# Kernel tuning notes

Hardware: AMD Instinct MI355X
Metric: run time of the kernel (lower is better)

Reference implementation:

```python
import jax, jax.numpy as jnp
import numpy as np

MODES1 = 12
MODES2 = 12
IN_CH = 32
OUT_CH = 32
B, H, W = 16, 256, 256
SCALE = 1.0 / (IN_CH * OUT_CH)


def setup_inputs() -> dict:
    key = jax.random.key(0)
    k1, k2, k3 = jax.random.split(key, 3)
    x = jax.random.normal(k1, (B, IN_CH, H, W), dtype=jnp.float32)
    w1 = SCALE * jax.random.uniform(k2, (IN_CH, OUT_CH, MODES1, MODES2, 2), dtype=jnp.float32)
    w2 = SCALE * jax.random.uniform(k3, (IN_CH, OUT_CH, MODES1, MODES2, 2), dtype=jnp.float32)
    return {"x": x, "weights1": w1, "weights2": w2}


def _compl_mul2d(inp, w):
    # inp: [b,i,x,y] complex ; w: [i,o,x,y,2] real -> complex
    wc = jax.lax.complex(w[..., 0], w[..., 1])
    return jnp.einsum('bixy,ioxy->boxy', inp, wc)


def reference(x, weights1, weights2):
    H_, W_ = x.shape[-2], x.shape[-1]
    m1 = min(MODES1, H_ // 2)
    m2 = min(MODES2, W_ // 2 + 1)
    x_ft = jnp.fft.rfft2(x.astype(jnp.float32))  # [B, Cin, H, W//2+1]
    low = _compl_mul2d(x_ft[:, :, :m1, :m2], weights1[:, :, :m1, :m2])
    high = _compl_mul2d(x_ft[:, :, -m1:, :m2], weights2[:, :, :m1, :m2])
    out_ft = jnp.zeros((x.shape[0], OUT_CH, H_, W_ // 2 + 1), dtype=jnp.complex64)
    out_ft = out_ft.at[:, :, :m1, :m2].set(low)
    out_ft = out_ft.at[:, :, H_ - m1:, :m2].set(high)
    return jnp.fft.irfft2(out_ft, s=(H_, W_)).astype(x.dtype)
```

## Files before the change

kernel.cpp:

```cpp
#include <hip/hip_runtime.h>


#define TPI 6.28318530717958647692f

__global__ __launch_bounds__(256, 2) void k12_hwdft(const float* __restrict__ x,
                                                    float* __restrict__ Xf) {
  __shared__ float2 step2[128];
  __shared__ float red[4 * 7 * 128];
  __shared__ float2 Ys2[13 * 129];
  const int blk = blockIdx.x;
  const int bi = blk >> 1, wh = blk & 1;
  const int t = threadIdx.x;
  const int q = t >> 6, l = t & 63;

  if (t < 128) {
    float s, c;
    sincosf(TPI * (float)t * (1.0f / 256.0f), &s, &c);
    step2[t] = make_float2(c, s);
  }
  __syncthreads();

  const float2* xp2 = reinterpret_cast<const float2*>(x + (size_t)bi * 65536 + wh * 128) + l;
  float2 aC[13], aS12[12];
#pragma unroll
  for (int j = 0; j < 13; j++) aC[j] = make_float2(0.f, 0.f);
#pragma unroll
  for (int j = 0; j < 12; j++) aS12[j] = make_float2(0.f, 0.f);

  const int h0 = q * 32;
#pragma unroll 2
  for (int hh = 0; hh < 32; hh++) {
    int h = h0 + hh;
    float2 xa = xp2[h * 128];
    float2 xb = xp2[(h + 128) * 128];
    float2 xe = make_float2(xa.x + xb.x, xa.y + xb.y);
    float2 xo = make_float2(xa.x - xb.x, xa.y - xb.y);
    aC[0].x += xe.x; aC[0].y += xe.y;
    float2 st = step2[h];
    float cj = st.x, sj = st.y;
#pragma unroll
    for (int jj = 0; jj < 12; jj++) {
      float2 xj = (jj & 1) ? xe : xo;
      aC[jj + 1].x = fmaf(xj.x, cj, aC[jj + 1].x);
      aC[jj + 1].y = fmaf(xj.y, cj, aC[jj + 1].y);
      aS12[jj].x = fmaf(xj.x, sj, aS12[jj].x);
      aS12[jj].y = fmaf(xj.y, sj, aS12[jj].y);
      if (jj < 11) {
        float nc = fmaf(cj, st.x, -(sj * st.y));
        float ns = fmaf(cj, st.y, sj * st.x);
        cj = nc; sj = ns;
      }
    }
  }

  for (int p = 0; p < 4; p++) {
    __syncthreads();
#pragma unroll
    for (int cc = 0; cc < 7; cc++) {
      int cls = p * 7 + cc;
      if (cls < 26) {
        int j = cls >> 1;
        float2 v;
        if (cls & 1) v = (j == 0) ? make_float2(0.f, 0.f) : aS12[j - 1];
        else v = aC[j];
        *reinterpret_cast<float2*>(&red[(q * 7 + cc) * 128 + 2 * l]) = v;
      }
    }
    __syncthreads();
    for (int idx = t; idx < 7 * 128; idx += 256) {
      int cc = idx >> 7, wl = idx & 127;
      int cls = p * 7 + cc;
      if (cls < 26) {
        float s = red[(0 * 7 + cc) * 128 + wl] + red[(1 * 7 + cc) * 128 + wl] +
                  red[(2 * 7 + cc) * 128 + wl] + red[(3 * 7 + cc) * 128 + wl];
        if (cls & 1) Ys2[(cls >> 1) * 129 + wl].y = s;
        else         Ys2[(cls >> 1) * 129 + wl].x = s;
      }
    }
  }
  __syncthreads();

  if (t < 156) {
    int j = t / 12, kx = t % 12;
    float cs, ss;
    {
      float s, c;
      sincosf(TPI * (float)kx * (1.0f / 256.0f), &s, &c);
      cs = c; ss = -s;
    }
    const float2* CS = &Ys2[j * 129];
    float pr = 1.0f, pi = 0.0f;
    float A = 0, B = 0, D = 0, E = 0;
#pragma unroll 4
    for (int w = 0; w < 128; w++) {
      float2 v = CS[w];
      A = fmaf(v.x, pr, A);
      B = fmaf(v.x, pi, B);
      D = fmaf(v.y, pr, D);
      E = fmaf(v.y, pi, E);
      float npr = pr * cs - pi * ss;
      float npi = pr * ss + pi * cs;
      pr = npr; pi = npi;
    }
    float sgn = (wh && (kx & 1)) ? -1.0f : 1.0f;
    A *= sgn; B *= sgn; D *= sgn; E *= sgn;
    float2* Xo = reinterpret_cast<float2*>(Xf) + (size_t)wh * 147456;
    size_t base = (size_t)kx * 512 + bi;
    if (j <= 11) Xo[(size_t)j * 6144 + base] = make_float2(A + E, B - D);
    if (j >= 1)  Xo[(size_t)(24 - j) * 6144 + base] = make_float2(A - E, B + D);
  }
}

__global__ __launch_bounds__(256) void k3_mix(const float* __restrict__ Xf,
                                              const float* __restrict__ w1,
                                              const float* __restrict__ w2,
                                              float* __restrict__ Ff) {
  __shared__ float Xs[1024];
  __shared__ float Ws[2048];
  int m = blockIdx.x;
  int ky = m / 12, kx = m % 12;
  int t = threadIdx.x;
  const float* Xsl = Xf + (size_t)m * 1024;
  for (int e = t; e < 1024; e += 256) Xs[e] = Xsl[e] + Xsl[e + 294912];
  const float* Wp = (ky < 12) ? w1 : w2;
  int myr = (ky < 12) ? ky : ky - 12;
  int woff = myr * 24 + kx * 2;
  for (int e = t; e < 1024; e += 256) {
    float2 wv = *reinterpret_cast<const float2*>(Wp + (size_t)e * 288 + woff);
    Ws[e * 2] = wv.x; Ws[e * 2 + 1] = wv.y;
  }
  __syncthreads();
  int o = t & 31, bh = t >> 5;
  float ar = 0, ai = 0, br = 0, bi_ = 0;
#pragma unroll
  for (int i = 0; i < 32; i++) {
    float wr = Ws[i * 64 + o * 2], wi = Ws[i * 64 + o * 2 + 1];
    float x1r = Xs[bh * 64 + i * 2], x1i = Xs[bh * 64 + i * 2 + 1];
    float x2r = Xs[(bh + 8) * 64 + i * 2], x2i = Xs[(bh + 8) * 64 + i * 2 + 1];
    ar = fmaf(x1r, wr, ar); ar = fmaf(-x1i, wi, ar);
    ai = fmaf(x1r, wi, ai); ai = fmaf(x1i, wr, ai);
    br = fmaf(x2r, wr, br); br = fmaf(-x2i, wi, br);
    bi_ = fmaf(x2r, wi, bi_); bi_ = fmaf(x2i, wr, bi_);
  }
  float scale = (kx == 0 ? 1.0f : 2.0f) * (1.0f / 65536.0f);
  float2* Fo = reinterpret_cast<float2*>(Ff) + (size_t)m * 512;
  Fo[(size_t)bh * 32 + o] = make_float2(ar * scale, ai * scale);
  Fo[(size_t)(bh + 8) * 32 + o] = make_float2(br * scale, bi_ * scale);
}

__global__ __launch_bounds__(256) void k45_inv(const float* __restrict__ Ff,
                                               float* __restrict__ out) {
  __shared__ float tw[128 * 27];
  __shared__ float PQ[13 * 12 * 4];
  __shared__ float Gs[256 * 24];
  const int bo = blockIdx.x;
  const int t = threadIdx.x;
  const int l = t & 63, wq = t >> 6;

  for (int e = t; e < 128 * 13; e += 256) {
    int h = e / 13, j = e % 13;
    float s, c;
    sincosf(TPI * (float)((h * j) & 255) * (1.0f / 256.0f), &s, &c);
    tw[h * 27 + 2 * j] = c;
    tw[h * 27 + 2 * j + 1] = s;
  }
  if (t < 156) {
    int j = t / 12, kx = t % 12;
    const float2* F2 = reinterpret_cast<const float2*>(Ff);
    float lr = 0, li = 0, hr = 0, hi = 0;
    if (j < 12) { float2 v = F2[((size_t)j * 12 + kx) * 512 + bo]; lr = v.x; li = v.y; }
    if (j > 0)  { float2 v = F2[((size_t)(24 - j) * 12 + kx) * 512 + bo]; hr = v.x; hi = v.y; }
    PQ[(j * 12 + kx) * 4 + 0] = lr + hr;
    PQ[(j * 12 + kx) * 4 + 1] = li + hi;
    PQ[(j * 12 + kx) * 4 + 2] = hi - li;
    PQ[(j * 12 + kx) * 4 + 3] = lr - hr;
  }
  __syncthreads();

  if (t < 192) {
    const int kx = t % 12, hq = t / 12;
    float Pr[13], Pi[13], Qr[13], Qi[13];
#pragma unroll
    for (int j = 0; j < 13; j++) {
      Pr[j] = PQ[(j * 12 + kx) * 4 + 0];
      Pi[j] = PQ[(j * 12 + kx) * 4 + 1];
      Qr[j] = PQ[(j * 12 + kx) * 4 + 2];
      Qi[j] = PQ[(j * 12 + kx) * 4 + 3];
    }
    for (int hh = 0; hh < 8; hh++) {
      int h = hh * 16 + hq;
      float Er = 0, Ei = 0, Or = 0, Oi = 0;
#pragma unroll
      for (int j = 0; j < 13; j++) {
        float c = tw[h * 27 + 2 * j], s = tw[h * 27 + 2 * j + 1];
        if (j & 1) {
          Or = fmaf(Pr[j], c, Or); Or = fmaf(Qr[j], s, Or);
          Oi = fmaf(Pi[j], c, Oi); Oi = fmaf(Qi[j], s, Oi);
        } else {
          Er = fmaf(Pr[j], c, Er); Er = fmaf(Qr[j], s, Er);
          Ei = fmaf(Pi[j], c, Ei); Ei = fmaf(Qi[j], s, Ei);
        }
      }
      Gs[h * 24 + 2 * kx] = Er + Or;
      Gs[h * 24 + 2 * kx + 1] = Ei + Oi;
      Gs[(h + 128) * 24 + 2 * kx] = Er - Or;
      Gs[(h + 128) * 24 + 2 * kx + 1] = Ei - Oi;
    }
  }

  float cA[12], sA[12], cB[12], sB[12];
#pragma unroll
  for (int kx = 1; kx < 12; kx++) {
    float s, c;
    __sincosf(TPI * (float)((kx * (2 * l)) & 255) * (1.0f / 256.0f), &s, &c);
    cA[kx] = c; sA[kx] = s;
    __sincosf(TPI * (float)((kx * (2 * l + 1)) & 255) * (1.0f / 256.0f), &s, &c);
    cB[kx] = c; sB[kx] = s;
  }
  __syncthreads();

  float* ob0 = out + ((size_t)bo * 256 + wq * 64) * 256;
  for (int rs = 0; rs < 64; rs++) {
    int rl = wq * 64 + rs;
    float g[24];
    const float4* gr4 = reinterpret_cast<const float4*>(&Gs[rl * 24]);
#pragma unroll
    for (int qq = 0; qq < 6; qq++) {
      float4 v = gr4[qq];
      g[4 * qq] = v.x; g[4 * qq + 1] = v.y; g[4 * qq + 2] = v.z; g[4 * qq + 3] = v.w;
    }
    float E0 = g[0], O0 = 0, E1 = g[0], O1 = 0;
#pragma unroll
    for (int kx = 1; kx < 12; kx++) {
      float ta = g[2 * kx] * cA[kx] - g[2 * kx + 1] * sA[kx];
      float tb = g[2 * kx] * cB[kx] - g[2 * kx + 1] * sB[kx];
      if (kx & 1) { O0 += ta; O1 += tb; } else { E0 += ta; E1 += tb; }
    }
    float* orow = ob0 + rs * 256;
    *reinterpret_cast<float2*>(&orow[2 * l]) = make_float2(E0 + O0, E1 + O1);
    *reinterpret_cast<float2*>(&orow[128 + 2 * l]) = make_float2(E0 - O0, E1 - O1);
  }
}

extern "C" void kernel_launch(void* const* d_in, const int* in_sizes, int n_in,
                              void* d_out, int out_size, void* d_ws, size_t ws_size,
                              hipStream_t stream) {
  const float* x = (const float*)d_in[0];
  const float* w1 = (const float*)d_in[1];
  const float* w2 = (const float*)d_in[2];
  float* out = (float*)d_out;
  float* ws = (float*)d_ws;

  float* Xf = ws;
  float* Ff = ws + 589824;

  k12_hwdft<<<1024, 256, 0, stream>>>(x, Xf);
  k3_mix<<<288, 256, 0, stream>>>(Xf, w1, w2, Ff);
  k45_inv<<<512, 256, 0, stream>>>(Ff, out);
}
```

Measured before the change: 81.69 us.

## Split forward DFT kernel into four W-quarters per image with rotation fixup

The forward truncated-DFT kernel now gives each block a 64-column quarter of the W axis instead of a 128-column half. Each thread holds scalar accumulators instead of float2 pairs, and launch bounds rise to 4 blocks per CU. This doubles the grid to 2048 blocks and roughly halves registers per thread to raise occupancy and latency hiding on the load-bound pass. The quarter offset is applied as a twiddle rotation by multiples of i, and the mix kernel now sums four partial spectra, so it reads more and needs a larger workspace.

```diff
diff --git a/kernel.cpp b/kernel.cpp
--- a/kernel.cpp
+++ b/kernel.cpp
@@ -3,13 +3,13 @@
 
 #define TPI 6.28318530717958647692f
 
-__global__ __launch_bounds__(256, 2) void k12_hwdft(const float* __restrict__ x,
+__global__ __launch_bounds__(256, 4) void k12_hwdft(const float* __restrict__ x,
                                                     float* __restrict__ Xf) {
   __shared__ float2 step2[128];
-  __shared__ float red[4 * 7 * 128];
-  __shared__ float2 Ys2[13 * 129];
+  __shared__ float red[4 * 7 * 64];
+  __shared__ float2 Ys2[13 * 65];
   const int blk = blockIdx.x;
-  const int bi = blk >> 1, wh = blk & 1;
+  const int bi = blk >> 2, wq = blk & 3;
   const int t = threadIdx.x;
   const int q = t >> 6, l = t & 63;
 
@@ -20,31 +20,28 @@
   }
   __syncthreads();
 
-  const float2* xp2 = reinterpret_cast<const float2*>(x + (size_t)bi * 65536 + wh * 128) + l;
-  float2 aC[13], aS12[12];
-#pragma unroll
-  for (int j = 0; j < 13; j++) aC[j] = make_float2(0.f, 0.f);
-#pragma unroll
-  for (int j = 0; j < 12; j++) aS12[j] = make_float2(0.f, 0.f);
+  const float* xp = x + (size_t)bi * 65536 + wq * 64 + l;
+  float aC[13], aS12[12];
+#pragma unroll
+  for (int j = 0; j < 13; j++) aC[j] = 0.0f;
+#pragma unroll
+  for (int j = 0; j < 12; j++) aS12[j] = 0.0f;
 
   const int h0 = q * 32;
 #pragma unroll 2
   for (int hh = 0; hh < 32; hh++) {
     int h = h0 + hh;
-    float2 xa = xp2[h * 128];
-    float2 xb = xp2[(h + 128) * 128];
-    float2 xe = make_float2(xa.x + xb.x, xa.y + xb.y);
-    float2 xo = make_float2(xa.x - xb.x, xa.y - xb.y);
-    aC[0].x += xe.x; aC[0].y += xe.y;
+    float xa = xp[h * 256];
+    float xb = xp[(h + 128) * 256];
+    float xe = xa + xb, xo = xa - xb;
+    aC[0] += xe;
     float2 st = step2[h];
     float cj = st.x, sj = st.y;
 #pragma unroll
     for (int jj = 0; jj < 12; jj++) {
-      float2 xj = (jj & 1) ? xe : xo;
-      aC[jj + 1].x = fmaf(xj.x, cj, aC[jj + 1].x);
-      aC[jj + 1].y = fmaf(xj.y, cj, aC[jj + 1].y);
-      aS12[jj].x = fmaf(xj.x, sj, aS12[jj].x);
-      aS12[jj].y = fmaf(xj.y, sj, aS12[jj].y);
+      float xj = (jj & 1) ? xe : xo;
+      aC[jj + 1] = fmaf(xj, cj, aC[jj + 1]);
+      aS12[jj] = fmaf(xj, sj, aS12[jj]);
       if (jj < 11) {
         float nc = fmaf(cj, st.x, -(sj * st.y));
         float ns = fmaf(cj, st.y, sj * st.x);
@@ -60,21 +57,21 @@
       int cls = p * 7 + cc;
       if (cls < 26) {
         int j = cls >> 1;
-        float2 v;
-        if (cls & 1) v = (j == 0) ? make_float2(0.f, 0.f) : aS12[j - 1];
+        float v;
+        if (cls & 1) v = (j == 0) ? 0.0f : aS12[j - 1];
         else v = aC[j];
-        *reinterpret_cast<float2*>(&red[(q * 7 + cc) * 128 + 2 * l]) = v;
+        red[(q * 7 + cc) * 64 + l] = v;
       }
     }
     __syncthreads();
-    for (int idx = t; idx < 7 * 128; idx += 256) {
-      int cc = idx >> 7, wl = idx & 127;
+    for (int idx = t; idx < 7 * 64; idx += 256) {
+      int cc = idx >> 6, wl = idx & 63;
       int cls = p * 7 + cc;
       if (cls < 26) {
-        float s = red[(0 * 7 + cc) * 128 + wl] + red[(1 * 7 + cc) * 128 + wl] +
-                  red[(2 * 7 + cc) * 128 + wl] + red[(3 * 7 + cc) * 128 + wl];
-        if (cls & 1) Ys2[(cls >> 1) * 129 + wl].y = s;
-        else         Ys2[(cls >> 1) * 129 + wl].x = s;
+        float s = red[(0 * 7 + cc) * 64 + wl] + red[(1 * 7 + cc) * 64 + wl] +
+                  red[(2 * 7 + cc) * 64 + wl] + red[(3 * 7 + cc) * 64 + wl];
+        if (cls & 1) Ys2[(cls >> 1) * 65 + wl].y = s;
+        else         Ys2[(cls >> 1) * 65 + wl].x = s;
       }
     }
   }
@@ -88,11 +85,11 @@
       sincosf(TPI * (float)kx * (1.0f / 256.0f), &s, &c);
       cs = c; ss = -s;
     }
-    const float2* CS = &Ys2[j * 129];
+    const float2* CS = &Ys2[j * 65];
     float pr = 1.0f, pi = 0.0f;
     float A = 0, B = 0, D = 0, E = 0;
 #pragma unroll 4
-    for (int w = 0; w < 128; w++) {
+    for (int w = 0; w < 64; w++) {
       float2 v = CS[w];
       A = fmaf(v.x, pr, A);
       B = fmaf(v.x, pi, B);
@@ -102,12 +99,17 @@
       float npi = pr * ss + pi * cs;
       pr = npr; pi = npi;
     }
-    float sgn = (wh && (kx & 1)) ? -1.0f : 1.0f;
-    A *= sgn; B *= sgn; D *= sgn; E *= sgn;
-    float2* Xo = reinterpret_cast<float2*>(Xf) + (size_t)wh * 147456;
+    float r0 = A + E, i0 = B - D;
+    float r1 = A - E, i1 = B + D;
+    int rot = (kx * wq) & 3;
+    float t0, t1;
+    if (rot == 1) { t0 = r0; r0 = i0; i0 = -t0; t1 = r1; r1 = i1; i1 = -t1; }
+    else if (rot == 2) { r0 = -r0; i0 = -i0; r1 = -r1; i1 = -i1; }
+    else if (rot == 3) { t0 = r0; r0 = -i0; i0 = t0; t1 = r1; r1 = -i1; i1 = t1; }
+    float2* Xo = reinterpret_cast<float2*>(Xf) + (size_t)wq * 147456;
     size_t base = (size_t)kx * 512 + bi;
-    if (j <= 11) Xo[(size_t)j * 6144 + base] = make_float2(A + E, B - D);
-    if (j >= 1)  Xo[(size_t)(24 - j) * 6144 + base] = make_float2(A - E, B + D);
+    if (j <= 11) Xo[(size_t)j * 6144 + base] = make_float2(r0, i0);
+    if (j >= 1)  Xo[(size_t)(24 - j) * 6144 + base] = make_float2(r1, i1);
   }
 }
 
@@ -121,7 +123,8 @@
   int ky = m / 12, kx = m % 12;
   int t = threadIdx.x;
   const float* Xsl = Xf + (size_t)m * 1024;
-  for (int e = t; e < 1024; e += 256) Xs[e] = Xsl[e] + Xsl[e + 294912];
+  for (int e = t; e < 1024; e += 256)
+    Xs[e] = Xsl[e] + Xsl[e + 294912] + Xsl[e + 589824] + Xsl[e + 884736];
   const float* Wp = (ky < 12) ? w1 : w2;
   int myr = (ky < 12) ? ky : ky - 12;
   int woff = myr * 24 + kx * 2;
@@ -252,9 +255,9 @@
   float* ws = (float*)d_ws;
 
   float* Xf = ws;
-  float* Ff = ws + 589824;
-
-  k12_hwdft<<<1024, 256, 0, stream>>>(x, Xf);
+  float* Ff = ws + 1179648;
+
+  k12_hwdft<<<2048, 256, 0, stream>>>(x, Xf);
   k3_mix<<<288, 256, 0, stream>>>(Xf, w1, w2, Ff);
   k45_inv<<<512, 256, 0, stream>>>(Ff, out);
 }
```

Result: slower. 88.14 us (+7.9%).
